# Kernel tuning notes

Measured on AMD Instinct MI355X. Metric: run time of the kernel, lower is better.

Reference implementation:

```python
import jax, jax.numpy as jnp
import numpy as np

H = 12          # num heads
D = 768         # embed dim
HD = D // H     # head dim
SCALE = HD ** -0.5
NEG = -(3.0 ** 39)  # matches torch's triu(1) * -3.0**39 mask value


def setup_inputs() -> dict:
    key = jax.random.key(0)
    ks = jax.random.split(key, 9)
    B, S = 4, 1024
    lim = 1.0 / np.sqrt(D)
    def lin(k):
        kw, kb = jax.random.split(k)
        W = jax.random.uniform(kw, (D, D), jnp.float32, -lim, lim)  # [out,in]
        b = jax.random.uniform(kb, (D,), jnp.float32, -lim, lim)
        return W, b
    Wq, bq = lin(ks[0]); Wk, bk = lin(ks[1]); Wv, bv = lin(ks[2]); Wo, bo = lin(ks[3])
    hidden_states = jax.random.normal(ks[4], (B, S, D), jnp.float32)
    return {"hidden_states": hidden_states,
            "Wq": Wq, "bq": bq, "Wk": Wk, "bk": bk,
            "Wv": Wv, "bv": bv, "Wo": Wo, "bo": bo}


def reference(hidden_states, Wq, bq, Wk, bk, Wv, bv, Wo, bo):
    B, S, _ = hidden_states.shape
    split = lambda x: x.reshape(B, S, H, HD).transpose(0, 2, 1, 3)  # [B,H,S,HD]
    q = split(hidden_states @ Wq.T + bq) * SCALE
    k = split(hidden_states @ Wk.T + bk)
    v = split(hidden_states @ Wv.T + bv)
    scores = jnp.einsum('bhqd,bhkd->bhqk', q, k)
    causal_mask = jnp.triu(jnp.full((S, S), NEG, hidden_states.dtype), k=1)
    scores = scores + causal_mask  # broadcast over [B,H]
    probs = jax.nn.softmax(scores, axis=-1)
    out = jnp.einsum('bhqk,bhkd->bhqd', probs, v)
    out = out.transpose(0, 2, 1, 3).reshape(B, S, H * HD)
    return out @ Wo.T + bo
```

## Files before the change

kernel.cpp:

```cpp
#include <hip/hip_runtime.h>

#define NH 12
#define DM 768
#define HD 64
#define BB 4
#define SS 1024
#define MTOT (BB*SS)
#define ATT_SCALE 0.125f
#define NEGMASK (-4.0525551530189755e18f)

typedef __attribute__((ext_vector_type(8))) short short8;
typedef __attribute__((ext_vector_type(4))) float floatx4;
typedef __attribute__((ext_vector_type(4))) unsigned short ushort4v;

__device__ __forceinline__ float bf2f(unsigned short u){
    union { unsigned int i; float f; } x; x.i = ((unsigned int)u) << 16; return x.f;
}
__device__ __forceinline__ unsigned short f2bf(float f){
    union { float f; unsigned int i; } x; x.f = f;
    unsigned int i = x.i;
    return (unsigned short)((i + 0x7FFFu + ((i >> 16) & 1u)) >> 16);
}

#define XQ4 (MTOT*DM/4)
#define WQ4 (DM*DM/4)

__global__ __launch_bounds__(256) void convert_bf16(
    const float* __restrict__ X,
    const float* __restrict__ Wq, const float* __restrict__ Wk,
    const float* __restrict__ Wv, const float* __restrict__ Wo,
    unsigned short* __restrict__ Xb,
    unsigned short* __restrict__ Wqb, unsigned short* __restrict__ Wkb,
    unsigned short* __restrict__ Wvb, unsigned short* __restrict__ Wob)
{
    const int idx = blockIdx.x * 256 + threadIdx.x;
    const float* s; unsigned short* d; int off;
    if (idx < XQ4) { s = X; d = Xb; off = idx; }
    else {
        const int r = idx - XQ4;
        const int wsel = r / WQ4;
        off = r - wsel * WQ4;
        s = (wsel==0)?Wq:(wsel==1)?Wk:(wsel==2)?Wv:Wo;
        d = (wsel==0)?Wqb:(wsel==1)?Wkb:(wsel==2)?Wvb:Wob;
    }
    const float4 v = ((const float4*)s)[off];
    ushort4v o;
    o[0] = f2bf(v.x); o[1] = f2bf(v.y); o[2] = f2bf(v.z); o[3] = f2bf(v.w);
    ((ushort4v*)d)[off] = o;
}

__global__ __launch_bounds__(256) void qkv_mfma(
    const unsigned short* __restrict__ Xb,
    const unsigned short* __restrict__ Wqb,
    const unsigned short* __restrict__ Wkb,
    const unsigned short* __restrict__ Wvb,
    const float* __restrict__ bq, const float* __restrict__ bk,
    const float* __restrict__ bv,
    unsigned short* __restrict__ qout,
    unsigned short* __restrict__ kout,
    unsigned short* __restrict__ vout)
{
    const int which = blockIdx.z;
    const int n0 = blockIdx.x * 64;
    const int m0 = blockIdx.y * 128;
    const unsigned short* W = (which==0) ? Wqb : (which==1) ? Wkb : Wvb;
    const float* bias = (which==0) ? bq : (which==1) ? bk : bv;
    const float scl = (which==0) ? ATT_SCALE : 1.0f;

    __shared__ unsigned short As[128*32];
    __shared__ unsigned short Bs[64*32];

    const int t = threadIdx.x;
    const int w = t >> 6, lane = t & 63;
    const int c = lane & 15, g = lane >> 4;
    const int wr = w >> 1, wc = w & 1;

    floatx4 acc[4][2] = {};

    const int srow = lane >> 2;
    const int ske  = (lane & 3) * 8;

    for (int k0 = 0; k0 < DM; k0 += 32) {
        __syncthreads();
        #pragma unroll
        for (int j = 0; j < 2; ++j) {
            const int row = w*32 + j*16 + srow;
            __builtin_amdgcn_global_load_lds(
                (const __attribute__((address_space(1))) unsigned int*)
                    (Xb + (size_t)(m0 + row) * DM + k0 + ske),
                (__attribute__((address_space(3))) unsigned int*)
                    (As + (w*32 + j*16) * 32),
                16, 0, 0);
        }
        {
            const int row = w*16 + srow;
            __builtin_amdgcn_global_load_lds(
                (const __attribute__((address_space(1))) unsigned int*)
                    (W + (size_t)(n0 + row) * DM + k0 + ske),
                (__attribute__((address_space(3))) unsigned int*)
                    (Bs + (w*16) * 32),
                16, 0, 0);
        }
        __syncthreads();

        short8 af[4], bfr[2];
        #pragma unroll
        for (int mi = 0; mi < 4; ++mi)
            af[mi] = *(const short8*)(As + (wr*64 + mi*16 + c)*32 + g*8);
        #pragma unroll
        for (int ni = 0; ni < 2; ++ni)
            bfr[ni] = *(const short8*)(Bs + (wc*32 + ni*16 + c)*32 + g*8);
        #pragma unroll
        for (int mi = 0; mi < 4; ++mi)
            #pragma unroll
            for (int ni = 0; ni < 2; ++ni)
                acc[mi][ni] = __builtin_amdgcn_mfma_f32_16x16x32_bf16(
                    af[mi], bfr[ni], acc[mi][ni], 0, 0, 0);
    }

    #pragma unroll
    for (int mi = 0; mi < 4; ++mi) {
        #pragma unroll
        for (int r = 0; r < 4; ++r) {
            const int m = m0 + wr*64 + mi*16 + g*4 + r;
            const int b = m >> 10, s = m & 1023;
            #pragma unroll
            for (int ni = 0; ni < 2; ++ni) {
                const int n = n0 + wc*32 + ni*16 + c;
                const int h = n >> 6, hd = n & 63;
                const float val = (acc[mi][ni][r] + bias[n]) * scl;
                if (which == 2)
                    vout[(((size_t)(b*NH + h))*HD + hd)*SS + s] = f2bf(val);
                else if (which == 1)
                    kout[(((size_t)(b*NH + h))*SS + s)*HD + hd] = f2bf(val);
                else
                    qout[(((size_t)(b*NH + h))*SS + s)*HD + hd] = f2bf(val);
            }
        }
    }
}

__device__ __forceinline__ void attn_load_frags(
    const unsigned short* __restrict__ Kp,
    const unsigned short* __restrict__ VTp,
    int k0, int c, int g, short8 (&kf)[4][2], short8 (&vf)[2][4])
{
    #pragma unroll
    for (int nf = 0; nf < 4; ++nf)
        #pragma unroll
        for (int st = 0; st < 2; ++st) {
            kf[nf][st] = *(const short8*)(Kp + (size_t)(k0 + nf*16 + c) * HD + g*8 + 32*st);
            vf[st][nf] = *(const short8*)(VTp + (size_t)(nf*16 + c) * SS + k0 + g*8 + 32*st);
        }
}

__device__ __forceinline__ void attn_process_tile(
    const short8 (&kf)[4][2], const short8 (&vf)[2][4], const short8 (&qf)[2],
    int k0, bool islast, int qg, int c, int g,
    float& m_c, float& l_c, floatx4 (&Oacc)[4],
    unsigned short* __restrict__ Pl)
{
    floatx4 S[4] = {};
    #pragma unroll
    for (int nf = 0; nf < 4; ++nf)
        #pragma unroll
        for (int st = 0; st < 2; ++st)
            S[nf] = __builtin_amdgcn_mfma_f32_16x16x32_bf16(kf[nf][st], qf[st], S[nf], 0, 0, 0);

    if (islast) {
        #pragma unroll
        for (int nf = 0; nf < 4; ++nf) {
            #pragma unroll
            for (int r = 0; r < 4; ++r) {
                const int key = k0 + nf*16 + g*4 + r;
                if (key > qg) S[nf][r] += NEGMASK;
            }
        }
    }

    float mx = -INFINITY;
    #pragma unroll
    for (int nf = 0; nf < 4; ++nf)
        #pragma unroll
        for (int r = 0; r < 4; ++r) mx = fmaxf(mx, S[nf][r]);
    mx = fmaxf(mx, __shfl_xor(mx, 16, 64));
    mx = fmaxf(mx, __shfl_xor(mx, 32, 64));
    const float mnew = fmaxf(m_c, mx);
    const float alpha = __expf(m_c - mnew);
    float sum = 0.0f;
    #pragma unroll
    for (int nf = 0; nf < 4; ++nf)
        #pragma unroll
        for (int r = 0; r < 4; ++r) {
            const float p = __expf(S[nf][r] - mnew);
            S[nf][r] = p;
            sum += p;
        }
    sum += __shfl_xor(sum, 16, 64);
    sum += __shfl_xor(sum, 32, 64);
    l_c = l_c * alpha + sum;
    m_c = mnew;
    #pragma unroll
    for (int nf = 0; nf < 4; ++nf)
        #pragma unroll
        for (int r = 0; r < 4; ++r) Oacc[nf][r] *= alpha;

    #pragma unroll
    for (int nf = 0; nf < 4; ++nf)
        #pragma unroll
        for (int r = 0; r < 4; ++r)
            Pl[c * 72 + nf*16 + g*4 + r] = f2bf(S[nf][r]);

    #pragma unroll
    for (int st = 0; st < 2; ++st) {
        const short8 pf = *(const short8*)(Pl + c * 72 + g*8 + 32*st);
        #pragma unroll
        for (int nf = 0; nf < 4; ++nf)
            Oacc[nf] = __builtin_amdgcn_mfma_f32_16x16x32_bf16(vf[st][nf], pf, Oacc[nf], 0, 0, 0);
    }
}

__global__ __launch_bounds__(64) void attn_mfma(
    const unsigned short* __restrict__ Q,
    const unsigned short* __restrict__ K,
    const unsigned short* __restrict__ VT,
    unsigned short* __restrict__ O)
{
    const int idx = blockIdx.x;
    const int bh  = idx % 48;
    const int z   = 63 - (idx / 48);
    const int q0  = z * 16;

    const unsigned short* Qp  = Q  + (size_t)bh * SS * HD;
    const unsigned short* Kp  = K  + (size_t)bh * SS * HD;
    const unsigned short* VTp = VT + (size_t)bh * HD * SS;

    __shared__ unsigned short Pl[16 * 72];

    const int lane = threadIdx.x;
    const int c    = lane & 15;
    const int g    = lane >> 4;
    const int qg   = q0 + c;

    short8 qf[2];
    #pragma unroll
    for (int st = 0; st < 2; ++st)
        qf[st] = *(const short8*)(Qp + (size_t)(q0 + c) * HD + g*8 + 32*st);

    floatx4 Oacc[4] = {};
    float m_c = -INFINITY, l_c = 0.0f;

    const int ntile = z/4 + 1;

    short8 ka[4][2], va[2][4], kb[4][2], vb[2][4];
    attn_load_frags(Kp, VTp, 0, c, g, ka, va);

    for (int kt = 0; kt < ntile; kt += 2) {
        if (kt + 1 < ntile)
            attn_load_frags(Kp, VTp, (kt+1)*64, c, g, kb, vb);
        attn_process_tile(ka, va, qf, kt*64, kt == ntile-1, qg, c, g, m_c, l_c, Oacc, Pl);
        if (kt + 1 >= ntile) break;
        if (kt + 2 < ntile)
            attn_load_frags(Kp, VTp, (kt+2)*64, c, g, ka, va);
        attn_process_tile(kb, vb, qf, (kt+1)*64, kt+1 == ntile-1, qg, c, g, m_c, l_c, Oacc, Pl);
    }

    const int b = bh / NH, h = bh % NH;
    const float inv = 1.0f / l_c;
    unsigned short* op = O + ((size_t)(b*SS + q0 + c))*DM + h*HD;
    #pragma unroll
    for (int nf = 0; nf < 4; ++nf) {
        ushort4v o4;
        #pragma unroll
        for (int r = 0; r < 4; ++r) o4[r] = f2bf(Oacc[nf][r] * inv);
        *(ushort4v*)(op + nf*16 + g*4) = o4;
    }
}

__global__ __launch_bounds__(256) void out_mfma(
    const unsigned short* __restrict__ A,
    const unsigned short* __restrict__ Wb,
    const float* __restrict__ bias,
    float* __restrict__ outf)
{
    const int n0 = blockIdx.x * 64;
    const int m0 = blockIdx.y * 128;

    __shared__ unsigned short As[128*32];
    __shared__ unsigned short Bs[64*32];

    const int t = threadIdx.x;
    const int w = t >> 6, lane = t & 63;
    const int c = lane & 15, g = lane >> 4;
    const int wr = w >> 1, wc = w & 1;

    floatx4 acc[4][2] = {};

    const int srow = lane >> 2;
    const int ske  = (lane & 3) * 8;

    for (int k0 = 0; k0 < DM; k0 += 32) {
        __syncthreads();
        #pragma unroll
        for (int j = 0; j < 2; ++j) {
            const int row = w*32 + j*16 + srow;
            __builtin_amdgcn_global_load_lds(
                (const __attribute__((address_space(1))) unsigned int*)
                    (A + (size_t)(m0 + row) * DM + k0 + ske),
                (__attribute__((address_space(3))) unsigned int*)
                    (As + (w*32 + j*16) * 32),
                16, 0, 0);
        }
        {
            const int row = w*16 + srow;
            __builtin_amdgcn_global_load_lds(
                (const __attribute__((address_space(1))) unsigned int*)
                    (Wb + (size_t)(n0 + row) * DM + k0 + ske),
                (__attribute__((address_space(3))) unsigned int*)
                    (Bs + (w*16) * 32),
                16, 0, 0);
        }
        __syncthreads();

        short8 af[4], bfr[2];
        #pragma unroll
        for (int mi = 0; mi < 4; ++mi)
            af[mi] = *(const short8*)(As + (wr*64 + mi*16 + c)*32 + g*8);
        #pragma unroll
        for (int ni = 0; ni < 2; ++ni)
            bfr[ni] = *(const short8*)(Bs + (wc*32 + ni*16 + c)*32 + g*8);
        #pragma unroll
        for (int mi = 0; mi < 4; ++mi)
            #pragma unroll
            for (int ni = 0; ni < 2; ++ni)
                acc[mi][ni] = __builtin_amdgcn_mfma_f32_16x16x32_bf16(
                    af[mi], bfr[ni], acc[mi][ni], 0, 0, 0);
    }

    #pragma unroll
    for (int mi = 0; mi < 4; ++mi) {
        #pragma unroll
        for (int r = 0; r < 4; ++r) {
            const int m = m0 + wr*64 + mi*16 + g*4 + r;
            #pragma unroll
            for (int ni = 0; ni < 2; ++ni) {
                const int n = n0 + wc*32 + ni*16 + c;
                outf[(size_t)m * DM + n] = acc[mi][ni][r] + bias[n];
            }
        }
    }
}

extern "C" void kernel_launch(void* const* d_in, const int* in_sizes, int n_in,
                              void* d_out, int out_size, void* d_ws, size_t ws_size,
                              hipStream_t stream) {
    const float* X  = (const float*)d_in[0];
    const float* Wq = (const float*)d_in[1];
    const float* bq = (const float*)d_in[2];
    const float* Wk = (const float*)d_in[3];
    const float* bk = (const float*)d_in[4];
    const float* Wv = (const float*)d_in[5];
    const float* bv = (const float*)d_in[6];
    const float* Wo = (const float*)d_in[7];
    const float* bo = (const float*)d_in[8];
    float* out = (float*)d_out;

    const size_t elems = (size_t)MTOT * DM;
    const size_t welems = (size_t)DM * DM;
    unsigned short* q    = (unsigned short*)d_ws;
    unsigned short* k    = q    + elems;
    unsigned short* vt   = k    + elems;
    unsigned short* attn = vt   + elems;
    unsigned short* xb   = attn + elems;
    unsigned short* wqb  = xb   + elems;
    unsigned short* wkb  = wqb  + welems;
    unsigned short* wvb  = wkb  + welems;
    unsigned short* wob  = wvb  + welems;

    convert_bf16<<<dim3((XQ4 + 4*WQ4) / 256), 256, 0, stream>>>(
        X, Wq, Wk, Wv, Wo, xb, wqb, wkb, wvb, wob);
    qkv_mfma<<<dim3(12, 32, 3), 256, 0, stream>>>(
        xb, wqb, wkb, wvb, bq, bk, bv, q, k, vt);
    attn_mfma<<<dim3(3072), 64, 0, stream>>>(q, k, vt, attn);
    out_mfma<<<dim3(12, 32), 256, 0, stream>>>(attn, wob, bo, out);
}
```

Before: 187.3 us.

## Share K/V tiles across four waves via swizzled LDS with direct global-to-LDS loads

The attention kernel moves from single-wave blocks over 16 query rows to 256-thread blocks over 64 query rows. K and V^T tiles are now staged once per block into double-buffered shared memory with global_load_lds and an XOR swizzle, instead of each wave loading them into registers. This cuts redundant global and L2 traffic for K/V by sharing each tile among four waves and frees registers. In exchange it adds a block barrier per tile and LDS fragment reads. It also relies on the barrier ordering the asynchronous LDS-DMA loads correctly.

```diff
diff --git a/kernel.cpp b/kernel.cpp
--- a/kernel.cpp
+++ b/kernel.cpp
@@ -140,32 +140,51 @@
     }
 }
 
-__device__ __forceinline__ void attn_load_frags(
+__device__ __forceinline__ void stage_tile(
     const unsigned short* __restrict__ Kp,
     const unsigned short* __restrict__ VTp,
-    int k0, int c, int g, short8 (&kf)[4][2], short8 (&vf)[2][4])
-{
-    #pragma unroll
-    for (int nf = 0; nf < 4; ++nf)
-        #pragma unroll
-        for (int st = 0; st < 2; ++st) {
-            kf[nf][st] = *(const short8*)(Kp + (size_t)(k0 + nf*16 + c) * HD + g*8 + 32*st);
-            vf[st][nf] = *(const short8*)(VTp + (size_t)(nf*16 + c) * SS + k0 + g*8 + 32*st);
-        }
+    int k0, int w, int lane,
+    unsigned short* __restrict__ Ks,
+    unsigned short* __restrict__ Vs)
+{
+    const int rsub = lane >> 3;
+    const int cc   = (lane & 7) ^ rsub;
+    #pragma unroll
+    for (int j = 0; j < 2; ++j) {
+        const int r = w*16 + j*8 + rsub;
+        __builtin_amdgcn_global_load_lds(
+            (const __attribute__((address_space(1))) unsigned int*)
+                (Kp + (size_t)(k0 + r) * HD + cc*8),
+            (__attribute__((address_space(3))) unsigned int*)
+                (Ks + (w*16 + j*8) * HD),
+            16, 0, 0);
+        __builtin_amdgcn_global_load_lds(
+            (const __attribute__((address_space(1))) unsigned int*)
+                (VTp + (size_t)r * SS + k0 + cc*8),
+            (__attribute__((address_space(3))) unsigned int*)
+                (Vs + (w*16 + j*8) * HD),
+            16, 0, 0);
+    }
 }
 
 __device__ __forceinline__ void attn_process_tile(
-    const short8 (&kf)[4][2], const short8 (&vf)[2][4], const short8 (&qf)[2],
+    const unsigned short* __restrict__ Ks,
+    const unsigned short* __restrict__ Vs,
+    const short8 (&qf)[2],
     int k0, bool islast, int qg, int c, int g,
     float& m_c, float& l_c, floatx4 (&Oacc)[4],
     unsigned short* __restrict__ Pl)
 {
     floatx4 S[4] = {};
     #pragma unroll
-    for (int nf = 0; nf < 4; ++nf)
-        #pragma unroll
-        for (int st = 0; st < 2; ++st)
-            S[nf] = __builtin_amdgcn_mfma_f32_16x16x32_bf16(kf[nf][st], qf[st], S[nf], 0, 0, 0);
+    for (int nf = 0; nf < 4; ++nf) {
+        const int row = nf*16 + c;
+        #pragma unroll
+        for (int st = 0; st < 2; ++st) {
+            const short8 kf = *(const short8*)(Ks + row*HD + (((g + 4*st) ^ (c & 7)) * 8));
+            S[nf] = __builtin_amdgcn_mfma_f32_16x16x32_bf16(kf, qf[st], S[nf], 0, 0, 0);
+        }
+    }
 
     if (islast) {
         #pragma unroll
@@ -215,12 +234,15 @@
     for (int st = 0; st < 2; ++st) {
         const short8 pf = *(const short8*)(Pl + c * 72 + g*8 + 32*st);
         #pragma unroll
-        for (int nf = 0; nf < 4; ++nf)
-            Oacc[nf] = __builtin_amdgcn_mfma_f32_16x16x32_bf16(vf[st][nf], pf, Oacc[nf], 0, 0, 0);
-    }
-}
-
-__global__ __launch_bounds__(64) void attn_mfma(
+        for (int nf = 0; nf < 4; ++nf) {
+            const int row = nf*16 + c;
+            const short8 vf = *(const short8*)(Vs + row*HD + (((g + 4*st) ^ (c & 7)) * 8));
+            Oacc[nf] = __builtin_amdgcn_mfma_f32_16x16x32_bf16(vf, pf, Oacc[nf], 0, 0, 0);
+        }
+    }
+}
+
+__global__ __launch_bounds__(256) void attn_mfma(
     const unsigned short* __restrict__ Q,
     const unsigned short* __restrict__ K,
     const unsigned short* __restrict__ VT,
@@ -228,46 +250,50 @@
 {
     const int idx = blockIdx.x;
     const int bh  = idx % 48;
-    const int z   = 63 - (idx / 48);
-    const int q0  = z * 16;
+    const int z   = 15 - (idx / 48);
+    const int q0  = z * 64;
 
     const unsigned short* Qp  = Q  + (size_t)bh * SS * HD;
     const unsigned short* Kp  = K  + (size_t)bh * SS * HD;
     const unsigned short* VTp = VT + (size_t)bh * HD * SS;
 
-    __shared__ unsigned short Pl[16 * 72];
-
-    const int lane = threadIdx.x;
+    __shared__ unsigned short Ks[2][64*HD];
+    __shared__ unsigned short Vs[2][64*HD];
+    __shared__ unsigned short Pl[4][16*72];
+
+    const int t    = threadIdx.x;
+    const int w    = t >> 6;
+    const int lane = t & 63;
     const int c    = lane & 15;
     const int g    = lane >> 4;
-    const int qg   = q0 + c;
+    const int qg   = q0 + w*16 + c;
 
     short8 qf[2];
     #pragma unroll
     for (int st = 0; st < 2; ++st)
-        qf[st] = *(const short8*)(Qp + (size_t)(q0 + c) * HD + g*8 + 32*st);
+        qf[st] = *(const short8*)(Qp + (size_t)qg * HD + g*8 + 32*st);
 
     floatx4 Oacc[4] = {};
     float m_c = -INFINITY, l_c = 0.0f;
 
-    const int ntile = z/4 + 1;
-
-    short8 ka[4][2], va[2][4], kb[4][2], vb[2][4];
-    attn_load_frags(Kp, VTp, 0, c, g, ka, va);
-
-    for (int kt = 0; kt < ntile; kt += 2) {
+    const int ntile = z + 1;
+
+    stage_tile(Kp, VTp, 0, w, lane, Ks[0], Vs[0]);
+    __syncthreads();
+
+    for (int kt = 0; kt < ntile; ++kt) {
+        const int cur = kt & 1;
         if (kt + 1 < ntile)
-            attn_load_frags(Kp, VTp, (kt+1)*64, c, g, kb, vb);
-        attn_process_tile(ka, va, qf, kt*64, kt == ntile-1, qg, c, g, m_c, l_c, Oacc, Pl);
-        if (kt + 1 >= ntile) break;
-        if (kt + 2 < ntile)
-            attn_load_frags(Kp, VTp, (kt+2)*64, c, g, ka, va);
-        attn_process_tile(kb, vb, qf, (kt+1)*64, kt+1 == ntile-1, qg, c, g, m_c, l_c, Oacc, Pl);
+            stage_tile(Kp, VTp, (kt+1)*64, w, lane, Ks[cur^1], Vs[cur^1]);
+        attn_process_tile(Ks[cur], Vs[cur], qf, kt*64, kt == ntile-1,
+                          qg, c, g, m_c, l_c, Oacc, Pl[w]);
+        if (kt + 1 < ntile)
+            __syncthreads();
     }
 
     const int b = bh / NH, h = bh % NH;
     const float inv = 1.0f / l_c;
-    unsigned short* op = O + ((size_t)(b*SS + q0 + c))*DM + h*HD;
+    unsigned short* op = O + ((size_t)(b*SS + qg))*DM + h*HD;
     #pragma unroll
     for (int nf = 0; nf < 4; ++nf) {
         ushort4v o4;
@@ -381,6 +407,6 @@
         X, Wq, Wk, Wv, Wo, xb, wqb, wkb, wvb, wob);
     qkv_mfma<<<dim3(12, 32, 3), 256, 0, stream>>>(
         xb, wqb, wkb, wvb, bq, bk, bv, q, k, vt);
-    attn_mfma<<<dim3(3072), 64, 0, stream>>>(q, k, vt, attn);
+    attn_mfma<<<dim3(768), 256, 0, stream>>>(q, k, vt, attn);
     out_mfma<<<dim3(12, 32), 256, 0, stream>>>(attn, wob, bo, out);
 }
```

After: 161.2 us. -14.0%, faster.
